# Kernel optimization log

Measured on AMD Instinct MI355X. Metric: run time of the kernel, lower is better.

The kernel has to match this reference:

```python
import jax, jax.numpy as jnp
import numpy as np

GROUPS = 32
GN_EPS = 1e-6
LN_EPS = 1e-5
HEADS = 8
DH = 40


def group_norm(x, w, b):
    # x: [B, C, H, W], GroupNorm over (C//GROUPS, H, W) within each group
    B, C, H, W = x.shape
    xg = x.reshape(B, GROUPS, C // GROUPS, H, W)
    mu = xg.mean(axis=(2, 3, 4), keepdims=True)
    var = xg.var(axis=(2, 3, 4), keepdims=True)
    xg = (xg - mu) * jax.lax.rsqrt(var + GN_EPS)
    return xg.reshape(B, C, H, W) * w[None, :, None, None] + b[None, :, None, None]


def layer_norm(x, w, b):
    mu = x.mean(axis=-1, keepdims=True)
    var = x.var(axis=-1, keepdims=True)
    return (x - mu) * jax.lax.rsqrt(var + LN_EPS) * w + b


def attention(x, ctx, wq, wk, wv, wo, bo):
    # x: [B, N, D], ctx: [B, M, Dc]; weights stored (in, out)
    B, N, _ = x.shape
    M = ctx.shape[1]
    q = (x @ wq).reshape(B, N, HEADS, DH)
    k = (ctx @ wk).reshape(B, M, HEADS, DH)
    v = (ctx @ wv).reshape(B, M, HEADS, DH)
    sim = jnp.einsum('bihd,bjhd->bhij', q, k) * (DH ** -0.5)
    attn = jax.nn.softmax(sim, axis=-1)
    out = jnp.einsum('bhij,bjhd->bihd', attn, v).reshape(B, N, HEADS * DH)
    return out @ wo + bo


def geglu_ff(x, w1, b1, w2, b2):
    h = x @ w1 + b1
    a, g = jnp.split(h, 2, axis=-1)
    return (a * jax.nn.gelu(g, approximate=False)) @ w2 + b2


def conv1x1(x, w, b):
    # w: [C_out, C_in]
    return jnp.einsum('bihw,oi->bohw', x, w) + b[None, :, None, None]


def reference(x, context, gn_w, gn_b, pin_w, pin_b,
              ln1_w, ln1_b, q1, k1, v1, o1_w, o1_b,
              ln2_w, ln2_b, q2, k2, v2, o2_w, o2_b,
              ln3_w, ln3_b, ff1_w, ff1_b, ff2_w, ff2_b,
              pout_w, pout_b):
    B, C, H, W = x.shape
    x_in = x
    h = group_norm(x, gn_w, gn_b)
    h = conv1x1(h, pin_w, pin_b)
    h = h.reshape(B, C, H * W).transpose(0, 2, 1)  # b (h w) c
    # BasicTransformerBlock
    h = attention(layer_norm(h, ln1_w, ln1_b), layer_norm(h, ln1_w, ln1_b), q1, k1, v1, o1_w, o1_b) + h
    h = attention(layer_norm(h, ln2_w, ln2_b), context, q2, k2, v2, o2_w, o2_b) + h
    h = geglu_ff(layer_norm(h, ln3_w, ln3_b), ff1_w, ff1_b, ff2_w, ff2_b) + h
    h = h.transpose(0, 2, 1).reshape(B, C, H, W)
    h = conv1x1(h, pout_w, pout_b)
    return h + x_in


def setup_inputs() -> dict:
    key = jax.random.key(0)
    ks = jax.random.split(key, 20)
    B, C, H, W = 1, 320, 64, 64
    CTX_N, CTX_D = 77, 768
    INNER, FFI = 320, 1280

    def n(k, shape, s=0.02):
        return jax.random.normal(k, shape, jnp.float32) * s

    return {
        'x': jax.random.normal(ks[0], (B, C, H, W), jnp.float32),
        'context': jax.random.normal(ks[1], (B, CTX_N, CTX_D), jnp.float32),
        'gn_w': jnp.ones((C,), jnp.float32), 'gn_b': jnp.zeros((C,), jnp.float32),
        'pin_w': n(ks[2], (INNER, C)), 'pin_b': jnp.zeros((INNER,), jnp.float32),
        'ln1_w': jnp.ones((INNER,), jnp.float32), 'ln1_b': jnp.zeros((INNER,), jnp.float32),
        'q1': n(ks[3], (INNER, INNER)), 'k1': n(ks[4], (INNER, INNER)), 'v1': n(ks[5], (INNER, INNER)),
        'o1_w': n(ks[6], (INNER, INNER)), 'o1_b': jnp.zeros((INNER,), jnp.float32),
        'ln2_w': jnp.ones((INNER,), jnp.float32), 'ln2_b': jnp.zeros((INNER,), jnp.float32),
        'q2': n(ks[7], (INNER, INNER)), 'k2': n(ks[8], (CTX_D, INNER)), 'v2': n(ks[9], (CTX_D, INNER)),
        'o2_w': n(ks[10], (INNER, INNER)), 'o2_b': jnp.zeros((INNER,), jnp.float32),
        'ln3_w': jnp.ones((INNER,), jnp.float32), 'ln3_b': jnp.zeros((INNER,), jnp.float32),
        'ff1_w': n(ks[11], (INNER, 2 * FFI)), 'ff1_b': jnp.zeros((2 * FFI,), jnp.float32),
        'ff2_w': n(ks[12], (FFI, INNER)), 'ff2_b': jnp.zeros((INNER,), jnp.float32),
        'pout_w': n(ks[13], (C, INNER)), 'pout_b': jnp.zeros((C,), jnp.float32),
    }
```

## Files before the change

kernel.cpp:

```cpp
#include <hip/hip_runtime.h>
#include <hip/hip_bf16.h>
#include <math.h>

#define N_SEQ  4096
#define DMODEL 320
#define NHEADS 8
#define DHEAD  40
#define CTXN   77
#define CTXD   768
#define FFI    1280

typedef short s8v __attribute__((ext_vector_type(8)));
typedef short s4v __attribute__((ext_vector_type(4)));
typedef float f4v __attribute__((ext_vector_type(4)));
typedef unsigned short u16;

static __device__ __forceinline__ u16 bf16u(float x) {
    unsigned u = __float_as_uint(x);
    return (u16)((u + 0x7FFFu + ((u >> 16) & 1u)) >> 16);
}
static __device__ __forceinline__ float b2f(u16 v) { return __uint_as_float((unsigned)v << 16); }
static __device__ __forceinline__ unsigned pack2(float a, float b) {
    return (unsigned)bf16u(a) | ((unsigned)bf16u(b) << 16);
}

#define GLD_LDS16(gp, lp) __builtin_amdgcn_global_load_lds( \
    (const __attribute__((address_space(1))) void*)(gp),    \
    (__attribute__((address_space(3))) void*)(lp), 16, 0, 0)

struct WC { const float* s; u16* d; int K, O, trans; };
struct WCs { WC a[12]; };
__global__ __launch_bounds__(256) void wcast2_k(WCs P) {
    __shared__ float tile[32][33];
    WC w = P.a[blockIdx.y];
    if (w.trans) {
        int ntk = w.K >> 5, nto = w.O >> 5;
        int tid = blockIdx.x;
        if (tid >= ntk * nto) return;
        int tk = tid % ntk, to = tid / ntk;
        int lr = threadIdx.x >> 5, lc = threadIdx.x & 31;
#pragma unroll
        for (int p = 0; p < 4; ++p) {
            int k = tk * 32 + p * 8 + lr;
            tile[p * 8 + lr][lc] = w.s[(size_t)k * w.O + to * 32 + lc];
        }
        __syncthreads();
#pragma unroll
        for (int p = 0; p < 4; ++p) {
            int o = to * 32 + p * 8 + lr;
            w.d[(size_t)o * w.K + tk * 32 + lc] = bf16u(tile[lc][p * 8 + lr]);
        }
    } else {
        int nel = w.K * w.O;
        for (int e = blockIdx.x * 256 + threadIdx.x; e < nel; e += gridDim.x * 256)
            w.d[e] = bf16u(w.s[e]);
    }
}

__global__ __launch_bounds__(256) void gn_stats_k(const float* __restrict__ x,
                                                  const float* __restrict__ gw, const float* __restrict__ gb,
                                                  float* __restrict__ sc, float* __restrict__ sh) {
    __shared__ float red[512];
    __shared__ float ms[2];
    int g = blockIdx.x, t = threadIdx.x;
    const float* xp = x + (size_t)g * 40960;
    float s = 0.f, ss = 0.f;
    for (int i = t; i < 40960; i += 256) { float v = xp[i]; s += v; ss += v * v; }
    red[t] = s; red[256 + t] = ss;
    __syncthreads();
    for (int st = 128; st > 0; st >>= 1) {
        if (t < st) { red[t] += red[t + st]; red[256 + t] += red[256 + t + st]; }
        __syncthreads();
    }
    if (t == 0) {
        float mean = red[0] / 40960.f;
        float var  = red[256] / 40960.f - mean * mean;
        ms[0] = mean; ms[1] = rsqrtf(var + 1e-6f);
    }
    __syncthreads();
    if (t < 10) {
        int c = g * 10 + t;
        float scv = gw[c] * ms[1];
        sc[c] = scv;
        sh[c] = gb[c] - ms[0] * scv;
    }
}

__global__ __launch_bounds__(256) void ln_stats_k(const float* __restrict__ in,
                                                  float* __restrict__ mu, float* __restrict__ rs) {
    int row = blockIdx.x * 4 + (threadIdx.x >> 6), l = threadIdx.x & 63;
    const float* p = in + (size_t)row * DMODEL;
    float s = 0.f, ss = 0.f;
#pragma unroll
    for (int j = 0; j < 5; ++j) { float v = p[l + 64 * j]; s += v; ss += v * v; }
    for (int o = 32; o > 0; o >>= 1) { s += __shfl_xor(s, o); ss += __shfl_xor(ss, o); }
    if (l == 0) {
        float mean = s * (1.f / 320.f);
        float var  = ss * (1.f / 320.f) - mean * mean;
        mu[row] = mean;
        rs[row] = rsqrtf(var + 1e-5f);
    }
}

struct GArg { const u16* Wt; const float* bias; float* outf; u16* outb; int ob_mode; };
#define GP 72
#define QSCALE 0.22811012f

template<int SITE>
__global__ __launch_bounds__(256) void gemm_t(const void* __restrict__ Av, int a_mode, int lda,
                                              const float* __restrict__ mu, const float* __restrict__ rs,
                                              const float* __restrict__ cw, const float* __restrict__ cb,
                                              GArg g0, GArg g1, GArg g2,
                                              const float* __restrict__ res,
                                              int Mrows, int K, int Oout, int obT_stride) {
    __shared__ __align__(16) u16 As[2][64 * GP];
    __shared__ __align__(16) u16 Wsm[2][64 * 64];
    const int t = threadIdx.x;
    const int w = t >> 6, lane = t & 63, c = lane & 15, quad = lane >> 4;
    const int o0 = blockIdx.x * 64, n0 = blockIdx.y * 64;
    GArg g = (blockIdx.z == 0) ? g0 : ((blockIdx.z == 1) ? g1 : g2);
    const f4v zero = {0.f, 0.f, 0.f, 0.f};
    f4v acc[4] = {zero, zero, zero, zero};
    const s8v z8 = {0, 0, 0, 0, 0, 0, 0, 0};
    const int nk = K >> 6;

    float fA[16];
    s8v bA0 = z8, bA1 = z8;

    const u16* gW0 = g.Wt + (size_t)(o0 + w * 16 + (lane >> 3)) * K + ((lane & 7) ^ (lane >> 3)) * 8;
    const u16* gW1 = gW0 + (size_t)8 * K;
    const int wdst = w * 1024;
    const int swb0 = 8 * (quad ^ (c & 7));
    const int swb1 = 8 * ((quad + 4) ^ (c & 7));

    auto gllW = [&](int b) {
        GLD_LDS16(gW0, &Wsm[b][wdst]);
        GLD_LDS16(gW1, &Wsm[b][wdst + 512]);
        gW0 += 64; gW1 += 64;
    };
    auto loadA = [&](int k0) {
        if (a_mode == 0) {
            const u16* A = (const u16*)Av;
            int i0 = t, i1 = t + 256;
            int nA = n0 + (i0 >> 3), nB = n0 + (i1 >> 3);
            bA0 = (nA < Mrows) ? *(const s8v*)(A + (size_t)nA * lda + k0 + (i0 & 7) * 8) : z8;
            bA1 = (nB < Mrows) ? *(const s8v*)(A + (size_t)nB * lda + k0 + (i1 & 7) * 8) : z8;
        } else if (a_mode == 1) {
            const float* A = (const float*)Av;
            int r = t >> 2, s16 = (t & 3) * 16;
            int n = n0 + r;
            if (n < Mrows) {
                const float* src = A + (size_t)n * lda + k0 + s16;
#pragma unroll
                for (int i = 0; i < 16; ++i) fA[i] = src[i];
            } else {
#pragma unroll
                for (int i = 0; i < 16; ++i) fA[i] = 0.f;
            }
        } else if (a_mode == 2) {
            const float* A = (const float*)Av;
#pragma unroll
            for (int j = 0; j < 16; ++j) {
                int e = t + 256 * j; int nn = e & 63, kk = e >> 6;
                int n = n0 + nn, kgl = k0 + kk;
                fA[j] = (n < Mrows) ? A[(size_t)kgl * lda + n] * cw[kgl] + cb[kgl] : 0.f;
            }
        } else if (a_mode == 3) {
            const float* A = (const float*)Av;
            int r = t >> 2, s16 = (t & 3) * 16;
            int n = n0 + r;
            if (n < Mrows) {
                const float* src = A + (size_t)n * lda + k0 + s16;
                const float* cwp = cw + k0 + s16;
                const float* cbp = cb + k0 + s16;
                float m_ = mu[n], rr = rs[n];
#pragma unroll
                for (int i = 0; i < 16; ++i) fA[i] = (src[i] - m_) * rr * cwp[i] + cbp[i];
            } else {
#pragma unroll
                for (int i = 0; i < 16; ++i) fA[i] = 0.f;
            }
        } else {
            const u16* Op = (const u16*)Av;
            const float* lp = mu;
            int r = t >> 2, s16 = (t & 3) * 16;
            int n = n0 + r;
            int ch0 = k0 + s16;
            int hdA = ch0 / 40;
            int hdB = (ch0 + 15) / 40;
            float invA = 1.f / (lp[(size_t)hdA * N_SEQ + n] + lp[(size_t)(8 + hdA) * N_SEQ + n]);
            float invB = (hdB == hdA) ? invA
                       : 1.f / (lp[(size_t)hdB * N_SEQ + n] + lp[(size_t)(8 + hdB) * N_SEQ + n]);
#pragma unroll
            for (int i = 0; i < 16; ++i) {
                int ch = ch0 + i;
                int hd = ch / 40;
                int d  = ch - hd * 40;
                float num = b2f(Op[((size_t)hd * N_SEQ + n) * DHEAD + d])
                          + b2f(Op[((size_t)(8 + hd) * N_SEQ + n) * DHEAD + d]);
                fA[i] = num * ((hd == hdA) ? invA : invB);
            }
        }
    };
    auto storeA = [&](int b) {
        if (a_mode == 0) {
            int i0 = t, i1 = t + 256;
            *(s8v*)&As[b][(i0 >> 3) * GP + (i0 & 7) * 8] = bA0;
            *(s8v*)&As[b][(i1 >> 3) * GP + (i1 & 7) * 8] = bA1;
        } else if (a_mode == 2) {
#pragma unroll
            for (int j = 0; j < 16; ++j) {
                int e = t + 256 * j; int nn = e & 63, kk = e >> 6;
                As[b][nn * GP + kk] = bf16u(fA[j]);
            }
        } else {
            int r = t >> 2, s16 = (t & 3) * 16;
            unsigned* dst = (unsigned*)&As[b][r * GP + s16];
#pragma unroll
            for (int i = 0; i < 8; ++i) dst[i] = pack2(fA[2 * i], fA[2 * i + 1]);
        }
    };

    gllW(0); loadA(0);
    storeA(0);
    __syncthreads();
    for (int k = 0; k < nk; ++k) {
        const int cur = k & 1;
        if (k + 1 < nk) { gllW(1 - cur); loadA((k + 1) << 6); }
        s8v a0 = *(const s8v*)&As[cur][(w * 16 + c) * GP + quad * 8];
        s8v a1 = *(const s8v*)&As[cur][(w * 16 + c) * GP + 32 + quad * 8];
#pragma unroll
        for (int nt = 0; nt < 4; ++nt) {
            s8v b0 = *(const s8v*)&Wsm[cur][(nt * 16 + c) * 64 + swb0];
            s8v b1 = *(const s8v*)&Wsm[cur][(nt * 16 + c) * 64 + swb1];
            acc[nt] = __builtin_amdgcn_mfma_f32_16x16x32_bf16(a0, b0, acc[nt], 0, 0, 0);
            acc[nt] = __builtin_amdgcn_mfma_f32_16x16x32_bf16(a1, b1, acc[nt], 0, 0, 0);
        }
        if (k + 1 < nk) { storeA(1 - cur); }
        __syncthreads();
    }
#pragma unroll
    for (int nt = 0; nt < 4; ++nt) {
        int o = o0 + nt * 16 + c;
        float vv[4];
#pragma unroll
        for (int r = 0; r < 4; ++r) vv[r] = acc[nt][r] + (g.bias ? g.bias[o] : 0.f);
        if (g.ob_mode == 3) {
            int nb = n0 + w * 16 + quad * 4;
            const float4 x4 = *(const float4*)(res + (size_t)o * obT_stride + nb);
            float4 o4 = make_float4(vv[0] + x4.x, vv[1] + x4.y, vv[2] + x4.z, vv[3] + x4.w);
            *(float4*)(g.outf + (size_t)o * obT_stride + nb) = o4;
        } else if (g.ob_mode == 4) {
#pragma unroll
            for (int r = 0; r < 4; ++r) {
                int n = n0 + w * 16 + quad * 4 + r;
                float vvv = vv[r];
                if (o < 320) vvv *= QSCALE;
                u16 bv = bf16u(vvv);
                if (o < 320)      g0.outb[(size_t)n * 320 + o] = bv;
                else if (o < 640) g1.outb[(size_t)n * 320 + (o - 320)] = bv;
                else              g2.outb[(size_t)(o - 640) * obT_stride + n] = bv;
            }
        } else {
#pragma unroll
            for (int r = 0; r < 4; ++r) {
                int n = n0 + w * 16 + quad * 4 + r;
                if (n >= Mrows) continue;
                float v = vv[r];
                if (res) v += res[(size_t)n * Oout + o];
                if (g.outf) g.outf[(size_t)n * Oout + o] = v;
                if (g.ob_mode == 1) g.outb[(size_t)n * Oout + o] = bf16u(v);
                else if (g.ob_mode == 2) g.outb[(size_t)o * obT_stride + n] = bf16u(v);
            }
        }
    }
}

__global__ __launch_bounds__(256) void gemm_gg(const float* __restrict__ A, int lda,
                                               const float* __restrict__ mu, const float* __restrict__ rs,
                                               const float* __restrict__ cw, const float* __restrict__ cb,
                                               const u16* __restrict__ Wt, const float* __restrict__ bias,
                                               u16* __restrict__ outb,
                                               int K, int Oout, int geglu_off) {
    __shared__ __align__(16) u16 As[64 * GP];
    __shared__ __align__(16) u16 Wsm[64 * GP];
    __shared__ __align__(16) u16 Wgm[64 * GP];
    const int t = threadIdx.x;
    const int w = t >> 6, lane = t & 63, c = lane & 15, quad = lane >> 4;
    const int o0 = blockIdx.x * 64, n0 = blockIdx.y * 64;
    const f4v zero = {0.f, 0.f, 0.f, 0.f};
    f4v acc[4]  = {zero, zero, zero, zero};
    f4v accg[4] = {zero, zero, zero, zero};
    const int nk = K >> 6;

    float fA[16];
    s8v wv0, wv1, gv0, gv1;

    auto loadWG = [&](int k0) {
        int i0 = t, i1 = t + 256;
        wv0 = *(const s8v*)(Wt + (size_t)(o0 + (i0 >> 3)) * K + k0 + (i0 & 7) * 8);
        wv1 = *(const s8v*)(Wt + (size_t)(o0 + (i1 >> 3)) * K + k0 + (i1 & 7) * 8);
        gv0 = *(const s8v*)(Wt + (size_t)(o0 + (i0 >> 3) + geglu_off) * K + k0 + (i0 & 7) * 8);
        gv1 = *(const s8v*)(Wt + (size_t)(o0 + (i1 >> 3) + geglu_off) * K + k0 + (i1 & 7) * 8);
    };
    auto storeWG = [&]() {
        int i0 = t, i1 = t + 256;
        *(s8v*)&Wsm[(i0 >> 3) * GP + (i0 & 7) * 8] = wv0;
        *(s8v*)&Wsm[(i1 >> 3) * GP + (i1 & 7) * 8] = wv1;
        *(s8v*)&Wgm[(i0 >> 3) * GP + (i0 & 7) * 8] = gv0;
        *(s8v*)&Wgm[(i1 >> 3) * GP + (i1 & 7) * 8] = gv1;
    };
    auto loadA = [&](int k0) {
        int r = t >> 2, s16 = (t & 3) * 16;
        int n = n0 + r;
        const float* src = A + (size_t)n * lda + k0 + s16;
        const float* cwp = cw + k0 + s16;
        const float* cbp = cb + k0 + s16;
        float m_ = mu[n], rr = rs[n];
#pragma unroll
        for (int i = 0; i < 16; ++i) fA[i] = (src[i] - m_) * rr * cwp[i] + cbp[i];
    };
    auto storeA = [&]() {
        int r = t >> 2, s16 = (t & 3) * 16;
        unsigned* dst = (unsigned*)&As[r * GP + s16];
#pragma unroll
        for (int i = 0; i < 8; ++i) dst[i] = pack2(fA[2 * i], fA[2 * i + 1]);
    };

    loadA(0); loadWG(0);
    storeA(); storeWG();
    __syncthreads();
    for (int k = 0; k < nk; ++k) {
        if (k + 1 < nk) { loadA((k + 1) << 6); loadWG((k + 1) << 6); }
        s8v a0 = *(const s8v*)&As[(w * 16 + c) * GP + quad * 8];
        s8v a1 = *(const s8v*)&As[(w * 16 + c) * GP + 32 + quad * 8];
#pragma unroll
        for (int nt = 0; nt < 4; ++nt) {
            s8v b0 = *(const s8v*)&Wsm[(nt * 16 + c) * GP + quad * 8];
            s8v b1 = *(const s8v*)&Wsm[(nt * 16 + c) * GP + 32 + quad * 8];
            acc[nt] = __builtin_amdgcn_mfma_f32_16x16x32_bf16(a0, b0, acc[nt], 0, 0, 0);
            acc[nt] = __builtin_amdgcn_mfma_f32_16x16x32_bf16(a1, b1, acc[nt], 0, 0, 0);
            s8v q0 = *(const s8v*)&Wgm[(nt * 16 + c) * GP + quad * 8];
            s8v q1 = *(const s8v*)&Wgm[(nt * 16 + c) * GP + 32 + quad * 8];
            accg[nt] = __builtin_amdgcn_mfma_f32_16x16x32_bf16(a0, q0, accg[nt], 0, 0, 0);
            accg[nt] = __builtin_amdgcn_mfma_f32_16x16x32_bf16(a1, q1, accg[nt], 0, 0, 0);
        }
        __syncthreads();
        if (k + 1 < nk) {
            storeA(); storeWG();
            __syncthreads();
        }
    }
#pragma unroll
    for (int nt = 0; nt < 4; ++nt) {
        int o = o0 + nt * 16 + c;
#pragma unroll
        for (int r = 0; r < 4; ++r) {
            int n = n0 + w * 16 + quad * 4 + r;
            float v = acc[nt][r] + bias[o];
            float gg = accg[nt][r] + bias[o + geglu_off];
            v = v * 0.5f * gg * (1.f + erff(gg * 0.70710678118654752f));
            outb[(size_t)n * Oout + o] = bf16u(v);
        }
    }
}

#define KSP 40
#define PSP 140
#define VP  136
__global__ __launch_bounds__(256) void attn_self8_k(const u16* __restrict__ qb, const u16* __restrict__ kb,
                                                    const u16* __restrict__ vt,
                                                    u16* __restrict__ Opart, float* __restrict__ lpart) {
    __shared__ __align__(16) u16 Ks[128 * KSP];
    __shared__ __align__(16) u16 Ps[64 * PSP];
    __shared__ __align__(16) u16 Vs[48 * VP];
    const int t = threadIdx.x;
    const int w = t >> 6, lane = t & 63, c = lane & 15, quad = lane >> 4;
    const int hd = blockIdx.y, ks = blockIdx.z;
    const int q0 = blockIdx.x * 64;
    const f4v zero = {0.f, 0.f, 0.f, 0.f};
    const s8v z8 = {0, 0, 0, 0, 0, 0, 0, 0};

    for (int i = t; i < 8 * VP / 2; i += 256) ((unsigned*)&Vs[40 * VP])[i] = 0u;
    __syncthreads();
    if (t < VP) Vs[40 * VP + t] = (u16)0x3F80;

    const u16* qrow = qb + (size_t)(q0 + w * 16 + c) * DMODEL + hd * DHEAD;
    s8v qa0 = *(const s8v*)(qrow + quad * 8);
    s8v qa1 = z8;
    if (quad == 0) qa1 = *(const s8v*)(qrow + 32);

    const int i0 = t, i1 = t + 256, i2 = t + 512;
    const int r0 = i0 / 5, s0 = i0 - r0 * 5;
    const int r1 = i1 / 5, s1 = i1 - r1 * 5;
    const int r2 = i2 / 5, s2 = i2 - r2 * 5;
    const u16* kq0 = kb + (size_t)(ks * 2048 + r0) * DMODEL + hd * DHEAD + s0 * 8;
    const u16* kq1 = kb + (size_t)(ks * 2048 + r1) * DMODEL + hd * DHEAD + s1 * 8;
    const u16* kq2 = kb + (size_t)(ks * 2048 + (t < 128 ? r2 : r0)) * DMODEL + hd * DHEAD + (t < 128 ? s2 : s0) * 8;
    u16* ksd0 = &Ks[r0 * KSP + s0 * 8];
    u16* ksd1 = &Ks[r1 * KSP + s1 * 8];
    u16* ksd2 = &Ks[(t < 128 ? r2 : r0) * KSP + (t < 128 ? s2 : s0) * 8];
    const int d0 = i0 >> 4, g0v = i0 & 15;
    const int d1 = i1 >> 4, g1v = i1 & 15;
    const int d2 = (t < 128 ? (i2 >> 4) : d0), g2v = (t < 128 ? (i2 & 15) : g0v);
    const u16* vq0 = vt + (size_t)(hd * DHEAD + d0) * N_SEQ + ks * 2048 + g0v * 8;
    const u16* vq1 = vt + (size_t)(hd * DHEAD + d1) * N_SEQ + ks * 2048 + g1v * 8;
    const u16* vq2 = vt + (size_t)(hd * DHEAD + d2) * N_SEQ + ks * 2048 + g2v * 8;
    u16* vsd0 = &Vs[d0 * VP + g0v * 8];
    u16* vsd1 = &Vs[d1 * VP + g1v * 8];
    u16* vsd2 = &Vs[d2 * VP + g2v * 8];
    const size_t kadv = (size_t)128 * DMODEL;

    s8v kA = *(const s8v*)kq0, kB = *(const s8v*)kq1, kC = *(const s8v*)kq2;
    s8v vA = *(const s8v*)vq0, vB = *(const s8v*)vq1, vC = *(const s8v*)vq2;
    kq0 += kadv; kq1 += kadv; kq2 += kadv;
    vq0 += 128;  vq1 += 128;  vq2 += 128;

    f4v o0 = zero, o1 = zero, o2 = zero;

    for (int kt = 0; kt < 16; ++kt) {
        __syncthreads();
        *(s8v*)ksd0 = kA; *(s8v*)ksd1 = kB;
        *(s8v*)vsd0 = vA; *(s8v*)vsd1 = vB;
        if (t < 128) { *(s8v*)ksd2 = kC; *(s8v*)vsd2 = vC; }
        if (kt + 1 < 16) {
            kA = *(const s8v*)kq0; kB = *(const s8v*)kq1;
            vA = *(const s8v*)vq0; vB = *(const s8v*)vq1;
            if (t < 128) { kC = *(const s8v*)kq2; vC = *(const s8v*)vq2; }
            kq0 += kadv; kq1 += kadv; kq2 += kadv;
            vq0 += 128;  vq1 += 128;  vq2 += 128;
        }
        __syncthreads();

        f4v sarr[8];
#pragma unroll
        for (int nt = 0; nt < 8; ++nt) {
            const int kr = nt * 16 + c;
            s8v b0 = *(const s8v*)&Ks[kr * KSP + quad * 8];
            s8v b1 = z8;
            if (quad == 0) b1 = *(const s8v*)&Ks[kr * KSP + 32];
            f4v s = __builtin_amdgcn_mfma_f32_16x16x32_bf16(qa0, b0, zero, 0, 0, 0);
            s = __builtin_amdgcn_mfma_f32_16x16x32_bf16(qa1, b1, s, 0, 0, 0);
            sarr[nt] = s;
        }

        u16* psw = &Ps[(size_t)(w * 16 + quad * 4) * PSP + c];
#pragma unroll
        for (int reg = 0; reg < 8; ++reg) {
            const int colb = (reg >> 2) * 64 + (reg & 3) * 16;
#pragma unroll
            for (int r = 0; r < 4; ++r) {
                float pv = exp2f(sarr[reg][r]);
                psw[r * PSP + colb] = (u16)(__float_as_uint(pv) >> 16);
            }
        }

        const u16* prow = &Ps[(size_t)(w * 16 + c) * PSP];
#pragma unroll
        for (int h2 = 0; h2 < 2; ++h2) {
            s8v pa0, pa1;
            {
                s4v lo = *(const s4v*)(prow + h2 * 64 + quad * 8);
                s4v hi = *(const s4v*)(prow + h2 * 64 + quad * 8 + 4);
                pa0 = (s8v){lo[0], lo[1], lo[2], lo[3], hi[0], hi[1], hi[2], hi[3]};
                s4v lo2 = *(const s4v*)(prow + h2 * 64 + 32 + quad * 8);
                s4v hi2 = *(const s4v*)(prow + h2 * 64 + 32 + quad * 8 + 4);
                pa1 = (s8v){lo2[0], lo2[1], lo2[2], lo2[3], hi2[0], hi2[1], hi2[2], hi2[3]};
            }
            {
                s8v v0 = *(const s8v*)&Vs[(0 * 16 + c) * VP + h2 * 64 + quad * 8];
                s8v v1 = *(const s8v*)&Vs[(0 * 16 + c) * VP + h2 * 64 + 32 + quad * 8];
                o0 = __builtin_amdgcn_mfma_f32_16x16x32_bf16(pa0, v0, o0, 0, 0, 0);
                o0 = __builtin_amdgcn_mfma_f32_16x16x32_bf16(pa1, v1, o0, 0, 0, 0);
            }
            {
                s8v v0 = *(const s8v*)&Vs[(1 * 16 + c) * VP + h2 * 64 + quad * 8];
                s8v v1 = *(const s8v*)&Vs[(1 * 16 + c) * VP + h2 * 64 + 32 + quad * 8];
                o1 = __builtin_amdgcn_mfma_f32_16x16x32_bf16(pa0, v0, o1, 0, 0, 0);
                o1 = __builtin_amdgcn_mfma_f32_16x16x32_bf16(pa1, v1, o1, 0, 0, 0);
            }
            {
                s8v v0 = *(const s8v*)&Vs[(2 * 16 + c) * VP + h2 * 64 + quad * 8];
                s8v v1 = *(const s8v*)&Vs[(2 * 16 + c) * VP + h2 * 64 + 32 + quad * 8];
                o2 = __builtin_amdgcn_mfma_f32_16x16x32_bf16(pa0, v0, o2, 0, 0, 0);
                o2 = __builtin_amdgcn_mfma_f32_16x16x32_bf16(pa1, v1, o2, 0, 0, 0);
            }
        }
    }

    const size_t pb = (size_t)(ks * 8 + hd) * N_SEQ;
#pragma unroll
    for (int r = 0; r < 4; ++r) {
        int q = q0 + w * 16 + quad * 4 + r;
        u16* op = Opart + (pb + q) * DHEAD;
        op[c]      = bf16u(o0[r]);
        op[16 + c] = bf16u(o1[r]);
        if (c < 8) op[32 + c] = bf16u(o2[r]);
        if (c == 8) lpart[pb + q] = o2[r];
    }
}

__global__ __launch_bounds__(256) void attn_cross3_k(const u16* __restrict__ qb,
                                                     const u16* __restrict__ kb,
                                                     const u16* __restrict__ vt,
                                                     u16* __restrict__ outb) {
    __shared__ __align__(16) u16 KsPs[64 * PSP];
    __shared__ __align__(16) u16 Vs[48 * VP];
    const int t = threadIdx.x;
    const int w = t >> 6, lane = t & 63, c = lane & 15, quad = lane >> 4;
    const int hd = blockIdx.y;
    const int q0 = blockIdx.x * 64;
    const float SC2 = 0.15811388300841897f * 1.4426950408889634f;
    const f4v zero = {0.f, 0.f, 0.f, 0.f};
    const s8v z8 = {0, 0, 0, 0, 0, 0, 0, 0};

    for (int i = t; i < 48 * VP / 2; i += 256) ((unsigned*)Vs)[i] = 0u;
    __syncthreads();
    if (t < VP) Vs[40 * VP + t] = (u16)0x3F80;
    for (int i = t; i < 400; i += 256) {
        int d = i / 10, kc = i - d * 10;
        s8v v = *(const s8v*)(vt + (size_t)(hd * DHEAD + d) * 128 + kc * 8);
        if (kc == 9) { v[5] = 0; v[6] = 0; v[7] = 0; }
        *(s8v*)&Vs[d * VP + kc * 8] = v;
    }
    for (int i = t; i < 385; i += 256) {
        int r = i / 5, sg = i - r * 5;
        *(s8v*)&KsPs[r * KSP + sg * 8] = *(const s8v*)(kb + (size_t)r * DMODEL + hd * DHEAD + sg * 8);
    }
    const u16* qrow = qb + (size_t)(q0 + w * 16 + c) * DMODEL + hd * DHEAD;
    s8v qa0 = *(const s8v*)(qrow + quad * 8);
    s8v qa1 = z8;
    if (quad == 0) qa1 = *(const s8v*)(qrow + 32);
    __syncthreads();

    f4v sarr[5];
#pragma unroll
    for (int nt = 0; nt < 5; ++nt) {
        const int kr = nt * 16 + c;
        s8v b0 = *(const s8v*)&KsPs[kr * KSP + quad * 8];
        s8v b1 = z8;
        if (quad == 0) b1 = *(const s8v*)&KsPs[kr * KSP + 32];
        f4v s = __builtin_amdgcn_mfma_f32_16x16x32_bf16(qa0, b0, zero, 0, 0, 0);
        s = __builtin_amdgcn_mfma_f32_16x16x32_bf16(qa1, b1, s, 0, 0, 0);
        sarr[nt] = s;
    }
    __syncthreads();

    u16* psw = &KsPs[(size_t)(w * 16 + quad * 4) * PSP + c];
#pragma unroll
    for (int r = 0; r < 4; ++r) {
        float s4 = (c < 13) ? sarr[4][r] : -1e30f;
        float mx = fmaxf(fmaxf(fmaxf(sarr[0][r], sarr[1][r]), fmaxf(sarr[2][r], sarr[3][r])), s4);
        mx = fmaxf(mx, __shfl_xor(mx, 1));
        mx = fmaxf(mx, __shfl_xor(mx, 2));
        mx = fmaxf(mx, __shfl_xor(mx, 4));
        mx = fmaxf(mx, __shfl_xor(mx, 8));
#pragma unroll
        for (int nt = 0; nt < 4; ++nt)
            psw[r * PSP + nt * 16] = bf16u(exp2f((sarr[nt][r] - mx) * SC2));
        psw[r * PSP + 64] = (c < 13) ? bf16u(exp2f((s4 - mx) * SC2)) : (u16)0;
        psw[r * PSP + 80] = 0;
    }

    const u16* prow = &KsPs[(size_t)(w * 16 + c) * PSP];
    f4v o0 = zero, o1 = zero, o2 = zero;
#pragma unroll
    for (int ch = 0; ch < 3; ++ch) {
        s4v lo = *(const s4v*)(prow + ch * 32 + quad * 8);
        s4v hi = *(const s4v*)(prow + ch * 32 + quad * 8 + 4);
        s8v pa = (s8v){lo[0], lo[1], lo[2], lo[3], hi[0], hi[1], hi[2], hi[3]};
        s8v v0 = *(const s8v*)&Vs[(0 * 16 + c) * VP + ch * 32 + quad * 8];
        o0 = __builtin_amdgcn_mfma_f32_16x16x32_bf16(pa, v0, o0, 0, 0, 0);
        s8v v1 = *(const s8v*)&Vs[(1 * 16 + c) * VP + ch * 32 + quad * 8];
        o1 = __builtin_amdgcn_mfma_f32_16x16x32_bf16(pa, v1, o1, 0, 0, 0);
        s8v v2 = *(const s8v*)&Vs[(2 * 16 + c) * VP + ch * 32 + quad * 8];
        o2 = __builtin_amdgcn_mfma_f32_16x16x32_bf16(pa, v2, o2, 0, 0, 0);
    }

#pragma unroll
    for (int r = 0; r < 4; ++r) {
        float inv = 1.f / __shfl(o2[r], (lane & 48) | 8);
        int q = q0 + w * 16 + quad * 4 + r;
        u16* op = outb + (size_t)q * DMODEL + hd * DHEAD;
        op[c]      = bf16u(o0[r] * inv);
        op[16 + c] = bf16u(o1[r] * inv);
        if (c < 8) op[32 + c] = bf16u(o2[r] * inv);
    }
}

extern "C" void kernel_launch(void* const* d_in, const int* in_sizes, int n_in,
                              void* d_out, int out_size, void* d_ws, size_t ws_size,
                              hipStream_t stream) {
    const float* x      = (const float*)d_in[0];
    const float* ctx    = (const float*)d_in[1];
    const float* gn_w   = (const float*)d_in[2];
    const float* gn_b   = (const float*)d_in[3];
    const float* pin_w  = (const float*)d_in[4];
    const float* pin_b  = (const float*)d_in[5];
    const float* ln1_w  = (const float*)d_in[6];
    const float* ln1_b  = (const float*)d_in[7];
    const float* q1     = (const float*)d_in[8];
    const float* k1     = (const float*)d_in[9];
    const float* v1     = (const float*)d_in[10];
    const float* o1_w   = (const float*)d_in[11];
    const float* o1_b   = (const float*)d_in[12];
    const float* ln2_w  = (const float*)d_in[13];
    const float* ln2_b  = (const float*)d_in[14];
    const float* q2     = (const float*)d_in[15];
    const float* k2     = (const float*)d_in[16];
    const float* v2     = (const float*)d_in[17];
    const float* o2_w   = (const float*)d_in[18];
    const float* o2_b   = (const float*)d_in[19];
    const float* ln3_w  = (const float*)d_in[20];
    const float* ln3_b  = (const float*)d_in[21];
    const float* ff1_w  = (const float*)d_in[22];
    const float* ff1_b  = (const float*)d_in[23];
    const float* ff2_w  = (const float*)d_in[24];
    const float* ff2_b  = (const float*)d_in[25];
    const float* pout_w = (const float*)d_in[26];
    const float* pout_b = (const float*)d_in[27];
    float* out = (float*)d_out;

    char* base = (char*)d_ws;
    float* h     = (float*)(base);
    u16*   qb16  = (u16*)(base + 5242880);
    u16*   kb16  = (u16*)(base + 7864320);
    u16*   vt16  = (u16*)(base + 10485760);
    u16*   ao16  = (u16*)(base + 13107200);
    u16*   ffg16 = (u16*)(base + 5242880);
    u16*   wbase = (u16*)(base + 15728640);
    u16* pinT  = wbase;
    u16* q1T   = pinT  + 102400;
    u16* k1T   = q1T   + 102400;
    u16* v1T   = k1T   + 102400;
    u16* o1T   = v1T   + 102400;
    u16* q2T   = o1T   + 102400;
    u16* o2T   = q2T   + 102400;
    u16* k2T   = o2T   + 102400;
    u16* v2T   = k2T   + 245760;
    u16* ff1T  = v2T   + 245760;
    u16* ff2T  = ff1T  + 819200;
    u16* poutT = ff2T  + 409600;
    float* lnmu = (float*)(base + 20807680);
    float* lnrs = lnmu + 4096;
    u16*   k2b16 = (u16*)(lnrs + 4096);
    u16*   v2t16 = (u16*)(lnrs + 4096 + 25600);
    u16*   Opart = (u16*)(lnrs + 4096 + 51200);
    float* lpart = (float*)(Opart + (size_t)2 * 8 * 4096 * 40);
    float* gnsc  = lpart + 2 * 8 * 4096;
    float* gnsh  = gnsc + 320;

    WCs wd;
    wd.a[0]  = {pin_w,  pinT,  320,  320,  0};
    wd.a[1]  = {q1,     q1T,   320,  320,  1};
    wd.a[2]  = {k1,     k1T,   320,  320,  1};
    wd.a[3]  = {v1,     v1T,   320,  320,  1};
    wd.a[4]  = {o1_w,   o1T,   320,  320,  1};
    wd.a[5]  = {q2,     q2T,   320,  320,  1};
    wd.a[6]  = {o2_w,   o2T,   320,  320,  1};
    wd.a[7]  = {k2,     k2T,   768,  320,  1};
    wd.a[8]  = {v2,     v2T,   768,  320,  1};
    wd.a[9]  = {ff1_w,  ff1T,  320,  2560, 1};
    wd.a[10] = {ff2_w,  ff2T,  1280, 320,  1};
    wd.a[11] = {pout_w, poutT, 320,  320,  0};
    wcast2_k<<<dim3(800, 12), 256, 0, stream>>>(wd);

    GArg gz = {nullptr, nullptr, nullptr, nullptr, 0};

    gn_stats_k<<<32, 256, 0, stream>>>(x, gn_w, gn_b, gnsc, gnsh);
    {
        GArg g0 = {pinT, pin_b, h, nullptr, 0};
        gemm_t<0><<<dim3(5, 64, 1), 256, 0, stream>>>(x, 2, 4096, nullptr, nullptr, gnsc, gnsh,
                                                      g0, gz, gz, nullptr, 4096, 320, 320, 0);
    }
    ln_stats_k<<<1024, 256, 0, stream>>>(h, lnmu, lnrs);
    {
        GArg g0 = {q1T, nullptr, nullptr, qb16, 4};
        GArg g1 = {nullptr, nullptr, nullptr, kb16, 0};
        GArg g2 = {nullptr, nullptr, nullptr, vt16, 0};
        gemm_t<1><<<dim3(15, 64, 1), 256, 0, stream>>>(h, 3, 320, lnmu, lnrs, ln1_w, ln1_b,
                                                       g0, g1, g2, nullptr, 4096, 320, 960, 4096);
    }
    attn_self8_k<<<dim3(64, 8, 2), 256, 0, stream>>>(qb16, kb16, vt16, Opart, lpart);
    {
        GArg g0 = {o1T, o1_b, h, nullptr, 0};
        gemm_t<2><<<dim3(5, 64, 1), 256, 0, stream>>>(Opart, 4, 0, lpart, nullptr, nullptr, nullptr,
                                                      g0, gz, gz, h, 4096, 320, 320, 0);
    }
    ln_stats_k<<<1024, 256, 0, stream>>>(h, lnmu, lnrs);
    {
        GArg g0 = {q2T, nullptr, nullptr, qb16, 1};
        gemm_t<3><<<dim3(5, 64, 1), 256, 0, stream>>>(h, 3, 320, lnmu, lnrs, ln2_w, ln2_b,
                                                      g0, gz, gz, nullptr, 4096, 320, 320, 0);
    }
    {
        GArg g0 = {k2T, nullptr, nullptr, k2b16, 1};
        GArg g1 = {v2T, nullptr, nullptr, v2t16, 2};
        gemm_t<4><<<dim3(5, 2, 2), 256, 0, stream>>>(ctx, 1, 768, nullptr, nullptr, nullptr, nullptr,
                                                     g0, g1, gz, nullptr, 77, 768, 320, 128);
    }
    attn_cross3_k<<<dim3(64, 8), 256, 0, stream>>>(qb16, k2b16, v2t16, ao16);
    {
        GArg g0 = {o2T, o2_b, h, nullptr, 0};
        gemm_t<5><<<dim3(5, 64, 1), 256, 0, stream>>>(ao16, 0, 320, nullptr, nullptr, nullptr, nullptr,
                                                      g0, gz, gz, h, 4096, 320, 320, 0);
    }
    ln_stats_k<<<1024, 256, 0, stream>>>(h, lnmu, lnrs);
    gemm_gg<<<dim3(20, 64, 1), 256, 0, stream>>>(h, 320, lnmu, lnrs, ln3_w, ln3_b,
                                                 ff1T, ff1_b, ffg16, 320, 1280, 1280);
    {
        GArg g0 = {ff2T, ff2_b, h, nullptr, 0};
        gemm_t<6><<<dim3(5, 64, 1), 256, 0, stream>>>(ffg16, 0, 1280, nullptr, nullptr, nullptr, nullptr,
                                                      g0, gz, gz, h, 4096, 1280, 320, 0);
    }
    {
        GArg g0 = {poutT, pout_b, out, nullptr, 3};
        gemm_t<7><<<dim3(5, 64, 1), 256, 0, stream>>>(h, 1, 320, nullptr, nullptr, nullptr, nullptr,
                                                      g0, gz, gz, x, 4096, 320, 320, 4096);
    }
}
```

Before: 436.2 us.

## Process 128 queries per attention block with 512 threads to share K/V tiles

The self-attention kernel now uses 8 waves and 128 query rows per block instead of 4 waves and 64 rows. Each K/V tile staged in shared memory is reused by twice as many queries, which halves global K/V traffic and halves the grid size. The cost is more shared memory per block for the larger P buffer, fewer blocks to spread across CUs, and heavier barriers with 512 threads.

New measurement: 421.3 us. 1.04x faster.

```diff
diff --git a/kernel.cpp b/kernel.cpp
--- a/kernel.cpp
+++ b/kernel.cpp
@@ -368,20 +368,20 @@
 #define KSP 40
 #define PSP 140
 #define VP  136
-__global__ __launch_bounds__(256) void attn_self8_k(const u16* __restrict__ qb, const u16* __restrict__ kb,
-                                                    const u16* __restrict__ vt,
-                                                    u16* __restrict__ Opart, float* __restrict__ lpart) {
+__global__ __launch_bounds__(512) void attn_self10_k(const u16* __restrict__ qb, const u16* __restrict__ kb,
+                                                     const u16* __restrict__ vt,
+                                                     u16* __restrict__ Opart, float* __restrict__ lpart) {
     __shared__ __align__(16) u16 Ks[128 * KSP];
-    __shared__ __align__(16) u16 Ps[64 * PSP];
+    __shared__ __align__(16) u16 Ps[128 * PSP];
     __shared__ __align__(16) u16 Vs[48 * VP];
     const int t = threadIdx.x;
     const int w = t >> 6, lane = t & 63, c = lane & 15, quad = lane >> 4;
     const int hd = blockIdx.y, ks = blockIdx.z;
-    const int q0 = blockIdx.x * 64;
+    const int q0 = blockIdx.x * 128;
     const f4v zero = {0.f, 0.f, 0.f, 0.f};
     const s8v z8 = {0, 0, 0, 0, 0, 0, 0, 0};
 
-    for (int i = t; i < 8 * VP / 2; i += 256) ((unsigned*)&Vs[40 * VP])[i] = 0u;
+    for (int i = t; i < 8 * VP / 2; i += 512) ((unsigned*)&Vs[40 * VP])[i] = 0u;
     __syncthreads();
     if (t < VP) Vs[40 * VP + t] = (u16)0x3F80;
 
@@ -390,45 +390,37 @@
     s8v qa1 = z8;
     if (quad == 0) qa1 = *(const s8v*)(qrow + 32);
 
-    const int i0 = t, i1 = t + 256, i2 = t + 512;
+    const int i0 = t, i2 = t + 512;
     const int r0 = i0 / 5, s0 = i0 - r0 * 5;
-    const int r1 = i1 / 5, s1 = i1 - r1 * 5;
-    const int r2 = i2 / 5, s2 = i2 - r2 * 5;
+    const int r2 = (t < 128) ? i2 / 5 : r0, s2 = (t < 128) ? (i2 - (i2 / 5) * 5) : s0;
     const u16* kq0 = kb + (size_t)(ks * 2048 + r0) * DMODEL + hd * DHEAD + s0 * 8;
-    const u16* kq1 = kb + (size_t)(ks * 2048 + r1) * DMODEL + hd * DHEAD + s1 * 8;
-    const u16* kq2 = kb + (size_t)(ks * 2048 + (t < 128 ? r2 : r0)) * DMODEL + hd * DHEAD + (t < 128 ? s2 : s0) * 8;
+    const u16* kq2 = kb + (size_t)(ks * 2048 + r2) * DMODEL + hd * DHEAD + s2 * 8;
     u16* ksd0 = &Ks[r0 * KSP + s0 * 8];
-    u16* ksd1 = &Ks[r1 * KSP + s1 * 8];
-    u16* ksd2 = &Ks[(t < 128 ? r2 : r0) * KSP + (t < 128 ? s2 : s0) * 8];
+    u16* ksd2 = &Ks[r2 * KSP + s2 * 8];
     const int d0 = i0 >> 4, g0v = i0 & 15;
-    const int d1 = i1 >> 4, g1v = i1 & 15;
-    const int d2 = (t < 128 ? (i2 >> 4) : d0), g2v = (t < 128 ? (i2 & 15) : g0v);
+    const int d2 = (t < 128) ? (i2 >> 4) : d0, g2v = (t < 128) ? (i2 & 15) : g0v;
     const u16* vq0 = vt + (size_t)(hd * DHEAD + d0) * N_SEQ + ks * 2048 + g0v * 8;
-    const u16* vq1 = vt + (size_t)(hd * DHEAD + d1) * N_SEQ + ks * 2048 + g1v * 8;
     const u16* vq2 = vt + (size_t)(hd * DHEAD + d2) * N_SEQ + ks * 2048 + g2v * 8;
     u16* vsd0 = &Vs[d0 * VP + g0v * 8];
-    u16* vsd1 = &Vs[d1 * VP + g1v * 8];
     u16* vsd2 = &Vs[d2 * VP + g2v * 8];
     const size_t kadv = (size_t)128 * DMODEL;
 
-    s8v kA = *(const s8v*)kq0, kB = *(const s8v*)kq1, kC = *(const s8v*)kq2;
-    s8v vA = *(const s8v*)vq0, vB = *(const s8v*)vq1, vC = *(const s8v*)vq2;
-    kq0 += kadv; kq1 += kadv; kq2 += kadv;
-    vq0 += 128;  vq1 += 128;  vq2 += 128;
+    s8v kA = *(const s8v*)kq0, kC = *(const s8v*)kq2;
+    s8v vA = *(const s8v*)vq0, vC = *(const s8v*)vq2;
+    kq0 += kadv; kq2 += kadv;
+    vq0 += 128;  vq2 += 128;
 
     f4v o0 = zero, o1 = zero, o2 = zero;
 
     for (int kt = 0; kt < 16; ++kt) {
         __syncthreads();
-        *(s8v*)ksd0 = kA; *(s8v*)ksd1 = kB;
-        *(s8v*)vsd0 = vA; *(s8v*)vsd1 = vB;
+        *(s8v*)ksd0 = kA; *(s8v*)vsd0 = vA;
         if (t < 128) { *(s8v*)ksd2 = kC; *(s8v*)vsd2 = vC; }
         if (kt + 1 < 16) {
-            kA = *(const s8v*)kq0; kB = *(const s8v*)kq1;
-            vA = *(const s8v*)vq0; vB = *(const s8v*)vq1;
+            kA = *(const s8v*)kq0; vA = *(const s8v*)vq0;
             if (t < 128) { kC = *(const s8v*)kq2; vC = *(const s8v*)vq2; }
-            kq0 += kadv; kq1 += kadv; kq2 += kadv;
-            vq0 += 128;  vq1 += 128;  vq2 += 128;
+            kq0 += kadv; kq2 += kadv;
+            vq0 += 128;  vq2 += 128;
         }
         __syncthreads();
 
@@ -681,7 +673,7 @@
         gemm_t<1><<<dim3(15, 64, 1), 256, 0, stream>>>(h, 3, 320, lnmu, lnrs, ln1_w, ln1_b,
                                                        g0, g1, g2, nullptr, 4096, 320, 960, 4096);
     }
-    attn_self8_k<<<dim3(64, 8, 2), 256, 0, stream>>>(qb16, kb16, vt16, Opart, lpart);
+    attn_self10_k<<<dim3(32, 8, 2), 512, 0, stream>>>(qb16, kb16, vt16, Opart, lpart);
     {
         GArg g0 = {o1T, o1_b, h, nullptr, 0};
         gemm_t<2><<<dim3(5, 64, 1), 256, 0, stream>>>(Opart, 4, 0, lpart, nullptr, nullptr, nullptr,
```
